# Performance work log

Hardware: AMD Instinct MI355X
Metric: run time of the kernel (lower is better)

## Reference

```python
import jax, jax.numpy as jnp
import numpy as np

S = 16384      # sequence length (tokens)
D = 400        # embedding_dim + char_embedding_dim = 300 + 100
H = 256        # hidden_dim // 2 per direction
T = 12         # tagset size
START, STOP = 10, 11
NEG = -10000.0


def setup_inputs() -> dict:
    key = jax.random.key(0)
    ks = jax.random.split(key, 30)
    rn = lambda k, shape, s=0.05: (jax.random.normal(k, shape, jnp.float32) * s)
    inp = {}
    inp['x'] = jax.random.normal(ks[0], (S, D), jnp.float32)
    inp['Wg'] = rn(ks[1], (2, D, D)); inp['bg'] = rn(ks[2], (2, D))
    inp['Wn'] = rn(ks[3], (2, D, D)); inp['bn'] = rn(ks[4], (2, D))
    inp['Wl'] = rn(ks[5], (2, D, D)); inp['bl'] = rn(ks[6], (2, D))
    inp['Wih0f'] = rn(ks[7], (4 * H, D));  inp['Whh0f'] = rn(ks[8], (4 * H, H));  inp['b0f'] = rn(ks[9], (4 * H,))
    inp['Wih0b'] = rn(ks[10], (4 * H, D)); inp['Whh0b'] = rn(ks[11], (4 * H, H)); inp['b0b'] = rn(ks[12], (4 * H,))
    inp['Wih1f'] = rn(ks[13], (4 * H, 2 * H)); inp['Whh1f'] = rn(ks[14], (4 * H, H)); inp['b1f'] = rn(ks[15], (4 * H,))
    inp['Wih1b'] = rn(ks[16], (4 * H, 2 * H)); inp['Whh1b'] = rn(ks[17], (4 * H, H)); inp['b1b'] = rn(ks[18], (4 * H,))
    inp['Wtag'] = rn(ks[19], (T, 2 * H)); inp['btag'] = rn(ks[20], (T,))
    trans = rn(ks[21], (T, T), 0.1)
    trans = trans.at[START, :].set(NEG).at[:, STOP].set(NEG)
    inp['transitions'] = trans
    inp['h0'] = rn(ks[22], (4, H), 1.0)  # (num_layers*2 directions, H)
    inp['c0'] = rn(ks[23], (4, H), 1.0)
    return inp


def _lstm_dir(xs, h0, c0, Wih, Whh, b, reverse):
    # PyTorch LSTM gate order: i, f, g, o
    def step(carry, xt):
        h, c = carry
        g = xt @ Wih.T + h @ Whh.T + b          # [4H]
        i, f, gg, o = jnp.split(g, 4)
        i = jax.nn.sigmoid(i); f = jax.nn.sigmoid(f)
        gg = jnp.tanh(gg); o = jax.nn.sigmoid(o)
        c = f * c + i * gg
        h = o * jnp.tanh(c)
        return (h, c), h
    _, hs = jax.lax.scan(step, (h0, c0), xs, reverse=reverse)
    return hs  # [S, H]


def _feats(x, Wg, bg, Wn, bn, Wl, bl,
           Wih0f, Whh0f, b0f, Wih0b, Whh0b, b0b,
           Wih1f, Whh1f, b1f, Wih1b, Whh1b, b1b,
           Wtag, btag, h0, c0):
    # Highway (2 layers, relu)
    for l in range(2):
        gate = jax.nn.sigmoid(x @ Wg[l].T + bg[l])
        x = gate * jax.nn.relu(x @ Wn[l].T + bn[l]) + (1.0 - gate) * (x @ Wl[l].T + bl[l])
    # 2-layer bidirectional LSTM (batch=1)
    hf = _lstm_dir(x, h0[0], c0[0], Wih0f, Whh0f, b0f, False)
    hb = _lstm_dir(x, h0[1], c0[1], Wih0b, Whh0b, b0b, True)
    x1 = jnp.concatenate([hf, hb], axis=-1)      # [S, 2H]
    hf = _lstm_dir(x1, h0[2], c0[2], Wih1f, Whh1f, b1f, False)
    hb = _lstm_dir(x1, h0[3], c0[3], Wih1b, Whh1b, b1b, True)
    lstm_out = jnp.concatenate([hf, hb], axis=-1)  # [S, 2H]
    return lstm_out @ Wtag.T + btag                # [S, T]


def _crf_log_partition(feats, transitions):
    init = jnp.full((T,), NEG, jnp.float32).at[START].set(0.0)
    def step(fv, feat):
        # tag_var[i, j] = fv[j] + transitions[i, j] + feat[i]
        tag_var = fv[None, :] + transitions + feat[:, None]
        return jax.scipy.special.logsumexp(tag_var, axis=1), None
    fv, _ = jax.lax.scan(step, init, feats)
    terminal = fv + transitions[STOP]
    return jax.scipy.special.logsumexp(terminal)


def reference(x, Wg, bg, Wn, bn, Wl, bl,
              Wih0f, Whh0f, b0f, Wih0b, Whh0b, b0b,
              Wih1f, Whh1f, b1f, Wih1b, Whh1b, b1b,
              Wtag, btag, transitions, h0, c0):
    feats = _feats(x, Wg, bg, Wn, bn, Wl, bl,
                   Wih0f, Whh0f, b0f, Wih0b, Whh0b, b0b,
                   Wih1f, Whh1f, b1f, Wih1b, Whh1b, b1b,
                   Wtag, btag, h0, c0)
    return _crf_log_partition(feats, transitions)
```

## Files before the change

kernel.cpp:

```cpp
#include <hip/hip_runtime.h>
#include <cstddef>

#define S_LEN 16384
#define DIM   400
#define HID   256
#define NTAG  12
#define TSTART 10
#define TSTOP  11
#define FNEG  -10000.0f

#define CHUNK_L 64
#define NCHUNK  256
#define WARM    16

typedef unsigned int   u32;
typedef unsigned short u16;
typedef _Float16 half2_t __attribute__((ext_vector_type(2)));
typedef short    short8 __attribute__((ext_vector_type(8)));
typedef float    f32x4  __attribute__((ext_vector_type(4)));
typedef unsigned short u16x4 __attribute__((ext_vector_type(4)));

__device__ __forceinline__ int sdot8f(u32 a, u32 b, int acc) {
#if defined(__has_builtin) && __has_builtin(__builtin_amdgcn_sdot8)
  return __builtin_amdgcn_sdot8((int)a, (int)b, acc, false);
#else
  #pragma unroll
  for (int i = 0; i < 8; ++i) {
    int ai = ((int)(a << (28 - 4 * i))) >> 28;
    int bi = ((int)(b << (28 - 4 * i))) >> 28;
    acc += ai * bi;
  }
  return acc;
#endif
}

__device__ __forceinline__ float sigmoidf_(float x) {
  return 1.0f / (1.0f + __expf(-x));
}
__device__ __forceinline__ float tanhf_(float x) {
  float e = __expf(2.0f * x);
  return 1.0f - 2.0f / (e + 1.0f);
}
__device__ __forceinline__ u16 f2bf(float f) {
  u32 u = __builtin_bit_cast(u32, f);
  u = u + 0x7FFFu + ((u >> 16) & 1u);
  return (u16)(u >> 16);
}

__global__ __launch_bounds__(256) void cvt_one(
    const float* __restrict__ in, u16* __restrict__ out, int n4)
{
  int i = blockIdx.x * 256 + threadIdx.x;
  if (i >= n4) return;
  float4 v = *(const float4*)(in + (size_t)i * 4);
  u16x4 o;
  o.x = f2bf(v.x); o.y = f2bf(v.y); o.z = f2bf(v.z); o.w = f2bf(v.w);
  *(u16x4*)(out + (size_t)i * 4) = o;
}

#define NCVT 8
__global__ __launch_bounds__(256) void cvt_multi(
    const float* __restrict__ s0, const float* __restrict__ s1,
    const float* __restrict__ s2, const float* __restrict__ s3,
    const float* __restrict__ s4, const float* __restrict__ s5,
    const float* __restrict__ s6, const float* __restrict__ s7,
    u16* __restrict__ d0, u16* __restrict__ d1,
    u16* __restrict__ d2, u16* __restrict__ d3,
    u16* __restrict__ d4, u16* __restrict__ d5,
    u16* __restrict__ d6, u16* __restrict__ d7,
    int n40, int n41, int n42, int n43, int n44, int n45, int n46, int n47)
{
  const int z = blockIdx.y;
  const float* src = (z==0)?s0:(z==1)?s1:(z==2)?s2:(z==3)?s3:(z==4)?s4:(z==5)?s5:(z==6)?s6:s7;
  u16* dst = (z==0)?d0:(z==1)?d1:(z==2)?d2:(z==3)?d3:(z==4)?d4:(z==5)?d5:(z==6)?d6:d7;
  const int n4 = (z==0)?n40:(z==1)?n41:(z==2)?n42:(z==3)?n43:(z==4)?n44:(z==5)?n45:(z==6)?n46:n47;
  int i = blockIdx.x * 256 + threadIdx.x;
  if (i >= n4) return;
  float4 v = *(const float4*)(src + (size_t)i * 4);
  u16x4 o;
  o.x = f2bf(v.x); o.y = f2bf(v.y); o.z = f2bf(v.z); o.w = f2bf(v.w);
  *(u16x4*)(dst + (size_t)i * 4) = o;
}

__global__ __launch_bounds__(256) void quant_whh4(
    const float* __restrict__ W0f, const float* __restrict__ W0b,
    const float* __restrict__ W1f, const float* __restrict__ W1b,
    const float* __restrict__ h0,
    u32* __restrict__ Wq4, float* __restrict__ Wsc,
    u32* __restrict__ h0q4, float* __restrict__ h0s)
{
  const int wave = threadIdx.x >> 6;
  const int lane = threadIdx.x & 63;
  const int row  = blockIdx.x * 4 + wave;
  if (row >= 4100) return;
  const float* src;
  if (row < 4096) {
    int mat = row >> 10, r = row & 1023;
    const float* W = (mat == 0) ? W0f : (mat == 1) ? W0b : (mat == 2) ? W1f : W1b;
    src = W + (size_t)r * HID;
  } else {
    src = h0 + (size_t)(row - 4096) * HID;
  }
  float4 v = *(const float4*)(src + lane * 4);
  float m = fmaxf(fmaxf(fabsf(v.x), fabsf(v.y)), fmaxf(fabsf(v.z), fabsf(v.w)));
#pragma unroll
  for (int off = 32; off; off >>= 1) m = fmaxf(m, __shfl_xor(m, off, 64));
  float inv   = (m > 0.f) ? 7.f / m : 0.f;
  float scale = (m > 0.f) ? m / 7.f : 0.f;
  int q0 = (int)rintf(v.x * inv);
  int q1 = (int)rintf(v.y * inv);
  int q2 = (int)rintf(v.z * inv);
  int q3 = (int)rintf(v.w * inv);
  u32 nib16 = (u32)(q0 & 15) | ((u32)(q1 & 15) << 4)
            | ((u32)(q2 & 15) << 8) | ((u32)(q3 & 15) << 12);
  u32 other = (u32)__shfl_xor((int)nib16, 1, 64);
  if ((lane & 1) == 0) {
    u32 word = nib16 | (other << 16);
    if (row < 4096) Wq4[(size_t)row * 32 + (lane >> 1)] = word;
    else            h0q4[(size_t)(row - 4096) * 32 + (lane >> 1)] = word;
  }
  if (lane == 0) {
    if (row < 4096) Wsc[row] = scale;
    else            h0s[row - 4096] = scale;
  }
}

__global__ __launch_bounds__(256) void hw_fused(
    const u16* __restrict__ A,
    const u16* __restrict__ Wgb, const u16* __restrict__ Wnb,
    const u16* __restrict__ Wlb,
    const float* __restrict__ bg, const float* __restrict__ bnn,
    const float* __restrict__ bl,
    u16* __restrict__ outb)
{
  __shared__ u16 As[128 * 40];
  __shared__ u16 Bs[3 * 64 * 40];
  const int tid  = threadIdx.x;
  const int bm0  = blockIdx.x * 128;
  const int bn0  = blockIdx.y * 64;
  const int w    = tid >> 6;
  const int lane = tid & 63;
  const int quad = lane >> 4;
  const int l16  = lane & 15;
  const int wm0  = (w >> 1) * 64;
  const int wn0  = (w & 1) * 32;
  const int K = DIM, N = DIM;

  f32x4 acc[3][4][2];
#pragma unroll
  for (int z = 0; z < 3; ++z)
#pragma unroll
    for (int i = 0; i < 4; ++i)
#pragma unroll
      for (int j = 0; j < 2; ++j) acc[z][i][j] = (f32x4){0.f, 0.f, 0.f, 0.f};

  short8 va[2], vb[3];
#pragma unroll
  for (int i = 0; i < 2; ++i) {
    int c = tid + i * 256, row = c >> 2, koff = (c & 3) * 8, gk = koff;
    va[i] = (short8){0,0,0,0,0,0,0,0};
    if (gk + 8 <= K)
      va[i] = *(const short8*)(A + (size_t)(bm0 + row) * K + gk);
  }
#pragma unroll
  for (int i = 0; i < 3; ++i) {
    int c = tid + i * 256, z = c >> 8, r = (c >> 2) & 63, koff = (c & 3) * 8;
    int gn = bn0 + r, gk = koff;
    const u16* W = (z == 0) ? Wgb : (z == 1) ? Wnb : Wlb;
    vb[i] = (short8){0,0,0,0,0,0,0,0};
    if (gn < N && gk + 8 <= K)
      vb[i] = *(const short8*)(W + (size_t)gn * K + gk);
  }

  for (int k0 = 0; k0 < K; k0 += 32) {
    __syncthreads();
#pragma unroll
    for (int i = 0; i < 2; ++i) {
      int c = tid + i * 256, row = c >> 2, koff = (c & 3) * 8;
      *(short8*)(&As[row * 40 + koff]) = va[i];
    }
#pragma unroll
    for (int i = 0; i < 3; ++i) {
      int c = tid + i * 256, z = c >> 8, r = (c >> 2) & 63, koff = (c & 3) * 8;
      *(short8*)(&Bs[z * 2560 + r * 40 + koff]) = vb[i];
    }
    __syncthreads();

    int kn = k0 + 32;
    if (kn < K) {
#pragma unroll
      for (int i = 0; i < 2; ++i) {
        int c = tid + i * 256, row = c >> 2, koff = (c & 3) * 8, gk = kn + koff;
        va[i] = (short8){0,0,0,0,0,0,0,0};
        if (gk + 8 <= K)
          va[i] = *(const short8*)(A + (size_t)(bm0 + row) * K + gk);
        else if (gk < K)
          for (int j = 0; j < K - gk; ++j) va[i][j] = (short)A[(size_t)(bm0 + row) * K + gk + j];
      }
#pragma unroll
      for (int i = 0; i < 3; ++i) {
        int c = tid + i * 256, z = c >> 8, r = (c >> 2) & 63, koff = (c & 3) * 8;
        int gn = bn0 + r, gk = kn + koff;
        const u16* W = (z == 0) ? Wgb : (z == 1) ? Wnb : Wlb;
        vb[i] = (short8){0,0,0,0,0,0,0,0};
        if (gn < N) {
          if (gk + 8 <= K)
            vb[i] = *(const short8*)(W + (size_t)gn * K + gk);
          else if (gk < K)
            for (int j = 0; j < K - gk; ++j) vb[i][j] = (short)W[(size_t)gn * K + gk + j];
        }
      }
    }

    short8 af[4];
#pragma unroll
    for (int mi = 0; mi < 4; ++mi)
      af[mi] = *(const short8*)(&As[(wm0 + mi * 16 + l16) * 40 + quad * 8]);
#pragma unroll
    for (int z = 0; z < 3; ++z) {
      short8 bf0 = *(const short8*)(&Bs[z * 2560 + (wn0 + l16) * 40 + quad * 8]);
      short8 bf1 = *(const short8*)(&Bs[z * 2560 + (wn0 + 16 + l16) * 40 + quad * 8]);
#pragma unroll
      for (int mi = 0; mi < 4; ++mi) {
        acc[z][mi][0] = __builtin_amdgcn_mfma_f32_16x16x32_bf16(af[mi], bf0, acc[z][mi][0], 0, 0, 0);
        acc[z][mi][1] = __builtin_amdgcn_mfma_f32_16x16x32_bf16(af[mi], bf1, acc[z][mi][1], 0, 0, 0);
      }
    }
  }

#pragma unroll
  for (int ni = 0; ni < 2; ++ni) {
    int n = bn0 + wn0 + ni * 16 + l16;
    if (n >= N) continue;
    float bgv = bg[n], bnv = bnn[n], blv = bl[n];
#pragma unroll
    for (int mi = 0; mi < 4; ++mi) {
#pragma unroll
      for (int r = 0; r < 4; ++r) {
        int m = bm0 + wm0 + mi * 16 + quad * 4 + r;
        float gv = acc[0][mi][ni][r] + bgv;
        float nv = acc[1][mi][ni][r] + bnv;
        float lv = acc[2][mi][ni][r] + blv;
        float g = sigmoidf_(gv);
        float v = g * fmaxf(nv, 0.f) + (1.f - g) * lv;
        outb[(size_t)m * N + n] = f2bf(v);
      }
    }
  }
}

__global__ __launch_bounds__(256) void gemm_multi(
    const u16* __restrict__ Ab,
    const u16* __restrict__ B0, const u16* __restrict__ B1,
    const float* __restrict__ bias0, const float* __restrict__ bias1,
    float* __restrict__ oF0, float* __restrict__ oF1,
    u16* __restrict__ oH, int pack4,
    int M, int N, int K)
{
  __shared__ u16 As[128 * 40];
  __shared__ u16 Bs[128 * 40];
  const int z = blockIdx.z;
  const u16* B      = (z == 0) ? B0 : B1;
  const float* bias = (z == 0) ? bias0 : bias1;
  float* outF       = (z == 0) ? oF0 : oF1;
  u16* outH         = pack4 ? (oH + (size_t)z * S_LEN * 1024) : nullptr;

  const int tid  = threadIdx.x;
  const int bm0  = blockIdx.x * 128;
  const int bn0  = blockIdx.y * 128;
  const int w    = tid >> 6;
  const int lane = tid & 63;
  const int quad = lane >> 4;
  const int l16  = lane & 15;
  const int wm0  = (w >> 1) * 64;
  const int wn0  = (w & 1) * 64;

  f32x4 acc[4][4];
#pragma unroll
  for (int i = 0; i < 4; ++i)
#pragma unroll
    for (int j = 0; j < 4; ++j) acc[i][j] = (f32x4){0.f, 0.f, 0.f, 0.f};

  short8 va[2], vb[2];
#pragma unroll
  for (int i = 0; i < 2; ++i) {
    int c = tid + i * 256, row = c >> 2, koff = (c & 3) * 8, gk = koff;
    int gn = bn0 + row;
    int brow = pack4 ? ((gn & 3) * 256 + (gn >> 2)) : gn;
    va[i] = (short8){0,0,0,0,0,0,0,0};
    vb[i] = (short8){0,0,0,0,0,0,0,0};
    if (gk + 8 <= K) {
      va[i] = *(const short8*)(Ab + (size_t)(bm0 + row) * K + gk);
      if (gn < N)
        vb[i] = *(const short8*)(B + (size_t)brow * K + gk);
    }
  }

  for (int k0 = 0; k0 < K; k0 += 32) {
    __syncthreads();
#pragma unroll
    for (int i = 0; i < 2; ++i) {
      int c = tid + i * 256, row = c >> 2, koff = (c & 3) * 8;
      *(short8*)(&As[row * 40 + koff]) = va[i];
      *(short8*)(&Bs[row * 40 + koff]) = vb[i];
    }
    __syncthreads();

    int kn = k0 + 32;
    if (kn < K) {
#pragma unroll
      for (int i = 0; i < 2; ++i) {
        int c = tid + i * 256, row = c >> 2, koff = (c & 3) * 8, gk = kn + koff;
        int gn = bn0 + row;
        int brow = pack4 ? ((gn & 3) * 256 + (gn >> 2)) : gn;
        va[i] = (short8){0,0,0,0,0,0,0,0};
        vb[i] = (short8){0,0,0,0,0,0,0,0};
        if (gk + 8 <= K) {
          va[i] = *(const short8*)(Ab + (size_t)(bm0 + row) * K + gk);
          if (gn < N)
            vb[i] = *(const short8*)(B + (size_t)brow * K + gk);
        } else if (gk < K) {
          for (int j = 0; j < K - gk; ++j) {
            va[i][j] = (short)Ab[(size_t)(bm0 + row) * K + gk + j];
            if (gn < N) vb[i][j] = (short)B[(size_t)brow * K + gk + j];
          }
        }
      }
    }

    short8 af[4], bf[4];
#pragma unroll
    for (int mi = 0; mi < 4; ++mi)
      af[mi] = *(const short8*)(&As[(wm0 + mi * 16 + l16) * 40 + quad * 8]);
#pragma unroll
    for (int ni = 0; ni < 4; ++ni)
      bf[ni] = *(const short8*)(&Bs[(wn0 + ni * 16 + l16) * 40 + quad * 8]);
#pragma unroll
    for (int mi = 0; mi < 4; ++mi)
#pragma unroll
      for (int ni = 0; ni < 4; ++ni)
        acc[mi][ni] = __builtin_amdgcn_mfma_f32_16x16x32_bf16(
            af[mi], bf[ni], acc[mi][ni], 0, 0, 0);
  }

#pragma unroll
  for (int mi = 0; mi < 4; ++mi) {
#pragma unroll
    for (int ni = 0; ni < 4; ++ni) {
      int n = bn0 + wn0 + ni * 16 + l16;
      if (n >= N) continue;
      float bv = 0.f;
      if (bias) bv = pack4 ? bias[(n & 3) * 256 + (n >> 2)] : bias[n];
#pragma unroll
      for (int r = 0; r < 4; ++r) {
        int m = bm0 + wm0 + mi * 16 + quad * 4 + r;
        float v = acc[mi][ni][r] + bv;
        if (pack4) {
          outH[(size_t)m * 1024 + n] = __builtin_bit_cast(u16, (_Float16)v);
        } else {
          outF[(size_t)m * N + n] = v;
        }
      }
    }
  }
}

__global__ __launch_bounds__(256) void lstm_scan(
    const u32* __restrict__ Wq4,
    const float* __restrict__ WscL,
    const u32* __restrict__ h0q4,
    const float* __restrict__ h0s,
    const float* __restrict__ c0,
    int row_base,
    const u16* __restrict__ P,
    u16* __restrict__ Xout)
{
  const int k    = blockIdx.x;
  const int dir  = blockIdx.y;
  const int j    = threadIdx.x;
  const int lane = j & 63;

  __shared__ u32 hq[2][32];

  const int out_lo = k * CHUNK_L;
  const int out_hi = out_lo + CHUNK_L - 1;
  int tstart, nsteps;
  bool real_init;
  if (dir == 0) {
    int wlo = out_lo - WARM; if (wlo < 0) wlo = 0;
    tstart = wlo;
    nsteps = out_hi - wlo + 1;
    real_init = (wlo == 0);
  } else {
    int whi = out_hi + WARM; if (whi > S_LEN - 1) whi = S_LEN - 1;
    tstart = whi;
    nsteps = whi - out_lo + 1;
    real_init = (whi == S_LEN - 1);
  }
  const int swrite = nsteps - CHUNK_L;

  u32 wi[32], wf[32], wg[32], wo[32];
  {
    const u32* base = Wq4 + (size_t)dir * 1024 * 32;
    const uint4* pi = (const uint4*)(base + (size_t)(j      ) * 32);
    const uint4* pf = (const uint4*)(base + (size_t)(j + 256) * 32);
    const uint4* pg = (const uint4*)(base + (size_t)(j + 512) * 32);
    const uint4* po = (const uint4*)(base + (size_t)(j + 768) * 32);
#pragma unroll
    for (int q = 0; q < 8; ++q) {
      uint4 a = pi[q], b = pf[q], c = pg[q], d = po[q];
      wi[4*q] = a.x; wi[4*q+1] = a.y; wi[4*q+2] = a.z; wi[4*q+3] = a.w;
      wf[4*q] = b.x; wf[4*q+1] = b.y; wf[4*q+2] = b.z; wf[4*q+3] = b.w;
      wg[4*q] = c.x; wg[4*q+1] = c.y; wg[4*q+2] = c.z; wg[4*q+3] = c.w;
      wo[4*q] = d.x; wo[4*q+1] = d.y; wo[4*q+2] = d.z; wo[4*q+3] = d.w;
    }
  }
  const float sci = WscL[dir * 1024 + j];
  const float scf = WscL[dir * 1024 + j + 256];
  const float scg = WscL[dir * 1024 + j + 512];
  const float sco = WscL[dir * 1024 + j + 768];

  float c_state = real_init ? c0[(row_base + dir) * HID + j] : 0.f;
  if (j < 32)
    hq[0][j] = real_init ? h0q4[(size_t)(row_base + dir) * 32 + j] : 0u;
  float hscale = real_init ? h0s[row_base + dir] : (1.f / 7.f);
  __syncthreads();

  const ptrdiff_t pstep = dir ? -1024 : 1024;
  const ptrdiff_t xstep = dir ? -512 : 512;
  const u16* pp = P + (size_t)dir * S_LEN * 1024 + (size_t)tstart * 1024 + j * 4;
  u16* xp = Xout + (size_t)tstart * 512 + dir * HID + j;

  uint2 p0 = *(const uint2*)pp;
  uint2 p1 = (nsteps > 1) ? *(const uint2*)(pp + pstep) : p0;
  const u16* pf2 = pp + 2 * pstep;

  int cur = 0;
  for (int s = 0; s < nsteps; ++s) {
    uint2 p2 = (s < nsteps - 2) ? *(const uint2*)pf2 : p1;
    pf2 += pstep;

    u32 hword = hq[cur][lane & 31];
    int ai = 0, af = 0, ag = 0, ao = 0;
#pragma unroll
    for (int q = 0; q < 32; ++q) {
      u32 hs = (u32)__builtin_amdgcn_readlane((int)hword, q);
      ai = sdot8f(wi[q], hs, ai);
      af = sdot8f(wf[q], hs, af);
      ag = sdot8f(wg[q], hs, ag);
      ao = sdot8f(wo[q], hs, ao);
    }
    half2_t pif = __builtin_bit_cast(half2_t, p0.x);
    half2_t pgo = __builtin_bit_cast(half2_t, p0.y);
    float gi = sigmoidf_((float)ai * (sci * hscale) + (float)pif[0]);
    float gf = sigmoidf_((float)af * (scf * hscale) + (float)pif[1]);
    float gg = tanhf_   ((float)ag * (scg * hscale) + (float)pgo[0]);
    float go = sigmoidf_((float)ao * (sco * hscale) + (float)pgo[1]);
    c_state = gf * c_state + gi * gg;
    float hv = go * tanhf_(c_state);

    int q4 = (int)rintf(hv * 7.f);
    u32 v = ((u32)(q4 & 15)) << (4 * (j & 7));
    v |= (u32)__shfl_xor((int)v, 1, 64);
    v |= (u32)__shfl_xor((int)v, 2, 64);
    v |= (u32)__shfl_xor((int)v, 4, 64);
    if ((j & 7) == 0) hq[cur ^ 1][j >> 3] = v;
    if (s >= swrite) *xp = f2bf(hv);

    hscale = 1.f / 7.f;
    p0 = p1; p1 = p2;
    xp += xstep;
    __syncthreads();
    cur ^= 1;
  }
}

__global__ __launch_bounds__(192) void crf_chunk(
    const float* __restrict__ feats, const float* __restrict__ trans,
    float* __restrict__ Mc)
{
  __shared__ float tr[144];
  __shared__ float fb[128][12];
  __shared__ float accA[156];
  __shared__ float accB[156];
  const int tid = threadIdx.x;
  const int cb  = blockIdx.x;
  if (tid < 144) tr[tid] = trans[tid];
  for (int i = tid; i < 128 * 12; i += 192)
    fb[i / 12][i % 12] = feats[(size_t)cb * 128 * 12 + i];
  __syncthreads();

  const int ii = tid / 12, jj = tid % 12;
  const bool act = tid < 144;
  float* cur = accA;
  float* nxt = accB;
  if (act) cur[ii * 13 + jj] = tr[ii * 12 + jj] + fb[0][ii];
  __syncthreads();

  for (int t = 1; t < 128; ++t) {
    if (act) {
      float v[12];
      float m = FNEG * 4.f;
#pragma unroll
      for (int kk = 0; kk < 12; ++kk) {
        v[kk] = tr[ii * 12 + kk] + cur[kk * 13 + jj];
        m = fmaxf(m, v[kk]);
      }
      float ssum = 0.f;
#pragma unroll
      for (int kk = 0; kk < 12; ++kk) ssum += __expf(v[kk] - m);
      nxt[ii * 13 + jj] = fb[t][ii] + m + __logf(ssum);
    }
    __syncthreads();
    float* tmp = cur; cur = nxt; nxt = tmp;
  }
  if (act) Mc[(size_t)cb * 144 + ii * 12 + jj] = cur[ii * 13 + jj];
}

__global__ __launch_bounds__(64) void crf_fold(
    const float* __restrict__ Mc, const float* __restrict__ trans,
    float* __restrict__ outp)
{
  __shared__ float fv[12];
  __shared__ float nf[12];
  const int tid = threadIdx.x;
  if (tid < 12) fv[tid] = (tid == TSTART) ? 0.f : FNEG;
  __syncthreads();
  for (int cidx = 0; cidx < 128; ++cidx) {
    if (tid < 12) {
      const float* M = Mc + (size_t)cidx * 144 + tid * 12;
      float v[12];
      float m = FNEG * 4.f;
#pragma unroll
      for (int j = 0; j < 12; ++j) {
        v[j] = M[j] + fv[j];
        m = fmaxf(m, v[j]);
      }
      float s = 0.f;
#pragma unroll
      for (int j = 0; j < 12; ++j) s += __expf(v[j] - m);
      nf[tid] = m + __logf(s);
    }
    __syncthreads();
    if (tid < 12) fv[tid] = nf[tid];
    __syncthreads();
  }
  if (tid == 0) {
    float v[12];
    float m = FNEG * 4.f;
#pragma unroll
    for (int i = 0; i < 12; ++i) {
      v[i] = fv[i] + trans[TSTOP * 12 + i];
      m = fmaxf(m, v[i]);
    }
    float s = 0.f;
#pragma unroll
    for (int i = 0; i < 12; ++i) s += __expf(v[i] - m);
    outp[0] = m + __logf(s);
  }
}

extern "C" void kernel_launch(void* const* d_in, const int* in_sizes, int n_in,
                              void* d_out, int out_size, void* d_ws, size_t ws_size,
                              hipStream_t stream)
{
  (void)in_sizes; (void)n_in; (void)out_size; (void)ws_size;
  const float* x     = (const float*)d_in[0];
  const float* Wg    = (const float*)d_in[1];
  const float* bg    = (const float*)d_in[2];
  const float* Wn    = (const float*)d_in[3];
  const float* bnn   = (const float*)d_in[4];
  const float* Wl    = (const float*)d_in[5];
  const float* bl    = (const float*)d_in[6];
  const float* Wih0f = (const float*)d_in[7];
  const float* Whh0f = (const float*)d_in[8];
  const float* b0f   = (const float*)d_in[9];
  const float* Wih0b = (const float*)d_in[10];
  const float* Whh0b = (const float*)d_in[11];
  const float* b0b   = (const float*)d_in[12];
  const float* Wih1f = (const float*)d_in[13];
  const float* Whh1f = (const float*)d_in[14];
  const float* b1f   = (const float*)d_in[15];
  const float* Wih1b = (const float*)d_in[16];
  const float* Whh1b = (const float*)d_in[17];
  const float* b1b   = (const float*)d_in[18];
  const float* Wtag  = (const float*)d_in[19];
  const float* btag  = (const float*)d_in[20];
  const float* trans = (const float*)d_in[21];
  const float* h0    = (const float*)d_in[22];
  const float* c0    = (const float*)d_in[23];

  char* ws = (char*)d_ws;
  size_t off = 0;
  auto alloc = [&](size_t bytes) -> void* {
    void* p = ws + off;
    off += (bytes + 255) & ~(size_t)255;
    return p;
  };
  u16* Pbuf = (u16*)alloc((size_t)2 * S_LEN * 1024 * 2);
  u16* X1b  = (u16*)alloc((size_t)S_LEN * 512 * 2);

  u16* xb      = (u16*)alloc((size_t)S_LEN * DIM * 2);
  u16* xhw1b   = (u16*)alloc((size_t)S_LEN * DIM * 2);
  u16* xhw2b   = (u16*)alloc((size_t)S_LEN * DIM * 2);
  u16* Wgb     = (u16*)alloc((size_t)2 * DIM * DIM * 2);
  u16* Wnb     = (u16*)alloc((size_t)2 * DIM * DIM * 2);
  u16* Wlb     = (u16*)alloc((size_t)2 * DIM * DIM * 2);
  u16* W0fb    = (u16*)alloc((size_t)1024 * DIM * 2);
  u16* W0bb    = (u16*)alloc((size_t)1024 * DIM * 2);
  u16* W1fb    = (u16*)alloc((size_t)1024 * 512 * 2);
  u16* W1bb    = (u16*)alloc((size_t)1024 * 512 * 2);
  u16* Wtagb   = (u16*)alloc((size_t)NTAG * 512 * 2);
  u32*   Wq4   = (u32*)alloc((size_t)4 * 1024 * 32 * 4);
  float* Wsc   = (float*)alloc((size_t)4096 * 4);
  u32*   h0q4b = (u32*)alloc((size_t)4 * 32 * 4);
  float* h0sb  = (float*)alloc((size_t)4 * 4);
  float* feats = (float*)alloc((size_t)S_LEN * NTAG * 4);
  float* Mc    = (float*)alloc((size_t)128 * 144 * 4);

  quant_whh4<<<1025, 256, 0, stream>>>(Whh0f, Whh0b, Whh1f, Whh1b, h0,
                                       Wq4, Wsc, h0q4b, h0sb);
  {
    int nx4 = S_LEN * DIM / 4;
    cvt_one<<<(nx4 + 255) / 256, 256, 0, stream>>>(x, xb, nx4);
    int nHW = 2 * DIM * DIM / 4;
    int nP0 = 1024 * DIM / 4;
    int nP1 = 1024 * 512 / 4;
    int nTG = NTAG * 512 / 4;
    dim3 gC((131072 + 255) / 256, NCVT);
    cvt_multi<<<gC, 256, 0, stream>>>(Wg, Wn, Wl, Wih0f, Wih0b, Wih1f, Wih1b, Wtag,
                                      Wgb, Wnb, Wlb, W0fb, W0bb, W1fb, W1bb, Wtagb,
                                      nHW, nHW, nHW, nP0, nP0, nP1, nP1, nTG);
  }

  dim3 gHW(S_LEN / 128, (DIM + 63) / 64);
  hw_fused<<<gHW, 256, 0, stream>>>(xb, Wgb, Wnb, Wlb, bg, bnn, bl, xhw1b);
  hw_fused<<<gHW, 256, 0, stream>>>(xhw1b, Wgb + 160000, Wnb + 160000,
                                    Wlb + 160000, bg + 400, bnn + 400, bl + 400,
                                    xhw2b);

  dim3 gP(S_LEN / 128, 1024 / 128, 2);
  gemm_multi<<<gP, 256, 0, stream>>>(xhw2b, W0fb, W0bb, b0f, b0b,
                                     nullptr, nullptr, Pbuf, 1,
                                     S_LEN, 1024, DIM);

  dim3 gS(NCHUNK, 2);
  lstm_scan<<<gS, 256, 0, stream>>>(Wq4, Wsc, h0q4b, h0sb, c0, 0, Pbuf, X1b);

  gemm_multi<<<gP, 256, 0, stream>>>(X1b, W1fb, W1bb, b1f, b1b,
                                     nullptr, nullptr, Pbuf, 1,
                                     S_LEN, 1024, 512);

  lstm_scan<<<gS, 256, 0, stream>>>(Wq4 + (size_t)2 * 1024 * 32, Wsc + 2048,
                                    h0q4b, h0sb, c0, 2, Pbuf, X1b);

  dim3 gT(S_LEN / 128, 1, 1);
  gemm_multi<<<gT, 256, 0, stream>>>(X1b, Wtagb, nullptr, btag, nullptr,
                                     feats, nullptr, nullptr, 0,
                                     S_LEN, NTAG, 512);

  crf_chunk<<<128, 192, 0, stream>>>(feats, trans, Mc);
  crf_fold<<<1, 64, 0, stream>>>(Mc, trans, (float*)d_out);
}
```

Measured before the change: 651.9 us.

## Double-buffer gemm_multi via direct global-to-LDS loads and pad K to 416

Rewrites the projection GEMM's staging to use global_load_lds direct copies into double-buffered LDS tiles, so the next k-slice loads while the current one feeds MFMAs and one barrier per iteration is dropped. The input-projection K dimension is zero-padded from 400 to 416, via a new pad-convert kernel for Wih0 and a padded second highway output, which removes the ragged tail path. The grid axes are also swapped so blocks sharing an A row tile run adjacently. The LDS row stride loses its 40-element padding, which may add bank conflicts on fragment reads.

```diff
diff --git a/kernel.cpp b/kernel.cpp
--- a/kernel.cpp
+++ b/kernel.cpp
@@ -3,6 +3,7 @@
 
 #define S_LEN 16384
 #define DIM   400
+#define DIMP  416
 #define HID   256
 #define NTAG  12
 #define TSTART 10
@@ -47,6 +48,12 @@
   return (u16)(u >> 16);
 }
 
+__device__ __forceinline__ void gl_lds16(const u16* g, u16* l) {
+  __builtin_amdgcn_global_load_lds(
+      (const __attribute__((address_space(1))) unsigned int*)g,
+      (__attribute__((address_space(3))) unsigned int*)l, 16, 0, 0);
+}
+
 __global__ __launch_bounds__(256) void cvt_one(
     const float* __restrict__ in, u16* __restrict__ out, int n4)
 {
@@ -56,6 +63,25 @@
   u16x4 o;
   o.x = f2bf(v.x); o.y = f2bf(v.y); o.z = f2bf(v.z); o.w = f2bf(v.w);
   *(u16x4*)(out + (size_t)i * 4) = o;
+}
+
+__global__ __launch_bounds__(256) void cvt_pad416(
+    const float* __restrict__ s0, const float* __restrict__ s1,
+    u16* __restrict__ d0, u16* __restrict__ d1)
+{
+  const float* src = blockIdx.y ? s1 : s0;
+  u16* dst = blockIdx.y ? d1 : d0;
+  int i = blockIdx.x * 256 + threadIdx.x;
+  const int total = 1024 * DIMP / 4;
+  if (i >= total) return;
+  int idx = i * 4;
+  int r = idx / DIMP, c = idx - r * DIMP;
+  u16x4 o = (u16x4){0, 0, 0, 0};
+  if (c < DIM) {
+    float4 v = *(const float4*)(src + (size_t)r * DIM + c);
+    o.x = f2bf(v.x); o.y = f2bf(v.y); o.z = f2bf(v.z); o.w = f2bf(v.w);
+  }
+  *(u16x4*)(dst + idx) = o;
 }
 
 #define NCVT 8
@@ -131,7 +157,7 @@
     const u16* __restrict__ Wlb,
     const float* __restrict__ bg, const float* __restrict__ bnn,
     const float* __restrict__ bl,
-    u16* __restrict__ outb)
+    u16* __restrict__ outb, int ostride, int opad)
 {
   __shared__ u16 As[128 * 40];
   __shared__ u16 Bs[3 * 64 * 40];
@@ -231,19 +257,25 @@
 #pragma unroll
   for (int ni = 0; ni < 2; ++ni) {
     int n = bn0 + wn0 + ni * 16 + l16;
-    if (n >= N) continue;
-    float bgv = bg[n], bnv = bnn[n], blv = bl[n];
+    if (n >= opad) continue;
+    bool val = n < N;
+    float bgv = val ? bg[n]  : 0.f;
+    float bnv = val ? bnn[n] : 0.f;
+    float blv = val ? bl[n]  : 0.f;
 #pragma unroll
     for (int mi = 0; mi < 4; ++mi) {
 #pragma unroll
       for (int r = 0; r < 4; ++r) {
         int m = bm0 + wm0 + mi * 16 + quad * 4 + r;
-        float gv = acc[0][mi][ni][r] + bgv;
-        float nv = acc[1][mi][ni][r] + bnv;
-        float lv = acc[2][mi][ni][r] + blv;
-        float g = sigmoidf_(gv);
-        float v = g * fmaxf(nv, 0.f) + (1.f - g) * lv;
-        outb[(size_t)m * N + n] = f2bf(v);
+        float v = 0.f;
+        if (val) {
+          float gv = acc[0][mi][ni][r] + bgv;
+          float nv = acc[1][mi][ni][r] + bnv;
+          float lv = acc[2][mi][ni][r] + blv;
+          float g = sigmoidf_(gv);
+          v = g * fmaxf(nv, 0.f) + (1.f - g) * lv;
+        }
+        outb[(size_t)m * ostride + n] = f2bf(v);
       }
     }
   }
@@ -257,8 +289,8 @@
     u16* __restrict__ oH, int pack4,
     int M, int N, int K)
 {
-  __shared__ u16 As[128 * 40];
-  __shared__ u16 Bs[128 * 40];
+  __shared__ u16 As[2][128 * 32];
+  __shared__ u16 Bs[2][128 * 32];
   const int z = blockIdx.z;
   const u16* B      = (z == 0) ? B0 : B1;
   const float* bias = (z == 0) ? bias0 : bias1;
@@ -266,8 +298,8 @@
   u16* outH         = pack4 ? (oH + (size_t)z * S_LEN * 1024) : nullptr;
 
   const int tid  = threadIdx.x;
-  const int bm0  = blockIdx.x * 128;
-  const int bn0  = blockIdx.y * 128;
+  const int bn0  = blockIdx.x * 128;
+  const int bm0  = blockIdx.y * 128;
   const int w    = tid >> 6;
   const int lane = tid & 63;
   const int quad = lane >> 4;
@@ -281,66 +313,41 @@
 #pragma unroll
     for (int j = 0; j < 4; ++j) acc[i][j] = (f32x4){0.f, 0.f, 0.f, 0.f};
 
-  short8 va[2], vb[2];
-#pragma unroll
-  for (int i = 0; i < 2; ++i) {
-    int c = tid + i * 256, row = c >> 2, koff = (c & 3) * 8, gk = koff;
-    int gn = bn0 + row;
-    int brow = pack4 ? ((gn & 3) * 256 + (gn >> 2)) : gn;
-    va[i] = (short8){0,0,0,0,0,0,0,0};
-    vb[i] = (short8){0,0,0,0,0,0,0,0};
-    if (gk + 8 <= K) {
-      va[i] = *(const short8*)(Ab + (size_t)(bm0 + row) * K + gk);
-      if (gn < N)
-        vb[i] = *(const short8*)(B + (size_t)brow * K + gk);
-    }
-  }
-
+  auto STAGE = [&](int buf, int k0) {
+#pragma unroll
+    for (int p = 0; p < 2; ++p) {
+      int c = (w * 2 + p) * 64 + lane;
+      int row = c >> 2, koff = (c & 3) * 8;
+      gl_lds16(Ab + (size_t)(bm0 + row) * K + k0 + koff,
+               &As[buf][(w * 2 + p) * 512]);
+      int gn = bn0 + row;
+      int brow = pack4 ? ((gn & 3) * 256 + (gn >> 2)) : (gn < N ? gn : 0);
+      gl_lds16(B + (size_t)brow * K + k0 + koff,
+               &Bs[buf][(w * 2 + p) * 512]);
+    }
+  };
+
+  STAGE(0, 0);
+  int cur = 0;
   for (int k0 = 0; k0 < K; k0 += 32) {
     __syncthreads();
-#pragma unroll
-    for (int i = 0; i < 2; ++i) {
-      int c = tid + i * 256, row = c >> 2, koff = (c & 3) * 8;
-      *(short8*)(&As[row * 40 + koff]) = va[i];
-      *(short8*)(&Bs[row * 40 + koff]) = vb[i];
-    }
-    __syncthreads();
-
     int kn = k0 + 32;
-    if (kn < K) {
-#pragma unroll
-      for (int i = 0; i < 2; ++i) {
-        int c = tid + i * 256, row = c >> 2, koff = (c & 3) * 8, gk = kn + koff;
-        int gn = bn0 + row;
-        int brow = pack4 ? ((gn & 3) * 256 + (gn >> 2)) : gn;
-        va[i] = (short8){0,0,0,0,0,0,0,0};
-        vb[i] = (short8){0,0,0,0,0,0,0,0};
-        if (gk + 8 <= K) {
-          va[i] = *(const short8*)(Ab + (size_t)(bm0 + row) * K + gk);
-          if (gn < N)
-            vb[i] = *(const short8*)(B + (size_t)brow * K + gk);
-        } else if (gk < K) {
-          for (int j = 0; j < K - gk; ++j) {
-            va[i][j] = (short)Ab[(size_t)(bm0 + row) * K + gk + j];
-            if (gn < N) vb[i][j] = (short)B[(size_t)brow * K + gk + j];
-          }
-        }
-      }
-    }
+    if (kn < K) STAGE(cur ^ 1, kn);
 
     short8 af[4], bf[4];
 #pragma unroll
     for (int mi = 0; mi < 4; ++mi)
-      af[mi] = *(const short8*)(&As[(wm0 + mi * 16 + l16) * 40 + quad * 8]);
+      af[mi] = *(const short8*)(&As[cur][(wm0 + mi * 16 + l16) * 32 + quad * 8]);
 #pragma unroll
     for (int ni = 0; ni < 4; ++ni)
-      bf[ni] = *(const short8*)(&Bs[(wn0 + ni * 16 + l16) * 40 + quad * 8]);
+      bf[ni] = *(const short8*)(&Bs[cur][(wn0 + ni * 16 + l16) * 32 + quad * 8]);
 #pragma unroll
     for (int mi = 0; mi < 4; ++mi)
 #pragma unroll
       for (int ni = 0; ni < 4; ++ni)
         acc[mi][ni] = __builtin_amdgcn_mfma_f32_16x16x32_bf16(
             af[mi], bf[ni], acc[mi][ni], 0, 0, 0);
+    cur ^= 1;
   }
 
 #pragma unroll
@@ -602,12 +609,12 @@
 
   u16* xb      = (u16*)alloc((size_t)S_LEN * DIM * 2);
   u16* xhw1b   = (u16*)alloc((size_t)S_LEN * DIM * 2);
-  u16* xhw2b   = (u16*)alloc((size_t)S_LEN * DIM * 2);
+  u16* xhw2b   = (u16*)alloc((size_t)S_LEN * DIMP * 2);
   u16* Wgb     = (u16*)alloc((size_t)2 * DIM * DIM * 2);
   u16* Wnb     = (u16*)alloc((size_t)2 * DIM * DIM * 2);
   u16* Wlb     = (u16*)alloc((size_t)2 * DIM * DIM * 2);
-  u16* W0fb    = (u16*)alloc((size_t)1024 * DIM * 2);
-  u16* W0bb    = (u16*)alloc((size_t)1024 * DIM * 2);
+  u16* W0fb    = (u16*)alloc((size_t)1024 * DIMP * 2);
+  u16* W0bb    = (u16*)alloc((size_t)1024 * DIMP * 2);
   u16* W1fb    = (u16*)alloc((size_t)1024 * 512 * 2);
   u16* W1bb    = (u16*)alloc((size_t)1024 * 512 * 2);
   u16* Wtagb   = (u16*)alloc((size_t)NTAG * 512 * 2);
@@ -623,26 +630,28 @@
   {
     int nx4 = S_LEN * DIM / 4;
     cvt_one<<<(nx4 + 255) / 256, 256, 0, stream>>>(x, xb, nx4);
+    dim3 gPad((1024 * DIMP / 4 + 255) / 256, 2);
+    cvt_pad416<<<gPad, 256, 0, stream>>>(Wih0f, Wih0b, W0fb, W0bb);
     int nHW = 2 * DIM * DIM / 4;
-    int nP0 = 1024 * DIM / 4;
     int nP1 = 1024 * 512 / 4;
     int nTG = NTAG * 512 / 4;
     dim3 gC((131072 + 255) / 256, NCVT);
     cvt_multi<<<gC, 256, 0, stream>>>(Wg, Wn, Wl, Wih0f, Wih0b, Wih1f, Wih1b, Wtag,
                                       Wgb, Wnb, Wlb, W0fb, W0bb, W1fb, W1bb, Wtagb,
-                                      nHW, nHW, nHW, nP0, nP0, nP1, nP1, nTG);
+                                      nHW, nHW, nHW, 0, 0, nP1, nP1, nTG);
   }
 
   dim3 gHW(S_LEN / 128, (DIM + 63) / 64);
-  hw_fused<<<gHW, 256, 0, stream>>>(xb, Wgb, Wnb, Wlb, bg, bnn, bl, xhw1b);
+  hw_fused<<<gHW, 256, 0, stream>>>(xb, Wgb, Wnb, Wlb, bg, bnn, bl,
+                                    xhw1b, DIM, DIM);
   hw_fused<<<gHW, 256, 0, stream>>>(xhw1b, Wgb + 160000, Wnb + 160000,
                                     Wlb + 160000, bg + 400, bnn + 400, bl + 400,
-                                    xhw2b);
-
-  dim3 gP(S_LEN / 128, 1024 / 128, 2);
+                                    xhw2b, DIMP, DIMP);
+
+  dim3 gP(1024 / 128, S_LEN / 128, 2);
   gemm_multi<<<gP, 256, 0, stream>>>(xhw2b, W0fb, W0bb, b0f, b0b,
                                      nullptr, nullptr, Pbuf, 1,
-                                     S_LEN, 1024, DIM);
+                                     S_LEN, 1024, DIMP);
 
   dim3 gS(NCHUNK, 2);
   lstm_scan<<<gS, 256, 0, stream>>>(Wq4, Wsc, h0q4b, h0sb, c0, 0, Pbuf, X1b);
@@ -654,7 +663,7 @@
   lstm_scan<<<gS, 256, 0, stream>>>(Wq4 + (size_t)2 * 1024 * 32, Wsc + 2048,
                                     h0q4b, h0sb, c0, 2, Pbuf, X1b);
 
-  dim3 gT(S_LEN / 128, 1, 1);
+  dim3 gT(1, S_LEN / 128, 1);
   gemm_multi<<<gT, 256, 0, stream>>>(X1b, Wtagb, nullptr, btag, nullptr,
                                      feats, nullptr, nullptr, 0,
                                      S_LEN, NTAG, 512);
```

After: 728.9 us. 11.8% more time.
